# Optimization experiments

Measured on AMD Instinct MI355X. Metric: run time of the kernel, lower is better.

## Reference

```python
import jax, jax.numpy as jnp
import numpy as np
from itertools import combinations_with_replacement

X_SIZE = 6        # dims of x
DEGREE = 2        # moment degree n
NPOINTS = 1_000_000
DIM_V = 28        # comb(X_SIZE + DEGREE, DEGREE)


def _veronese_indices(d, n):
    # monomials of total degree exactly n over homogeneous coords [1, x_1..x_d]
    combos = list(combinations_with_replacement(range(d + 1), n))  # [D_v, n]
    return np.asarray(combos, dtype=np.int32)


def generate_veronese(x, n):
    # x: [dims, npoints] -> v: [D_v, npoints], all monomials of degree <= n in x
    d, N = x.shape
    xh = jnp.concatenate([jnp.ones((1, N), x.dtype), x], axis=0)  # [d+1, N]
    idx = _veronese_indices(d, n)
    v = xh[idx[:, 0]]                 # [D_v, N]
    for k in range(1, n):             # n is tiny (2); fixed small loop
        v = v * xh[idx[:, k]]
    return v


def setup_inputs() -> dict:
    key = jax.random.key(0)
    k1, k2 = jax.random.split(key)
    x = jax.random.normal(k1, (NPOINTS, X_SIZE), dtype=jnp.float32)
    A = jax.random.normal(k2, (DIM_V, DIM_V), dtype=jnp.float32) / DIM_V
    M_inv = A @ A.T + jnp.eye(DIM_V, dtype=jnp.float32)  # SPD, like an inverse moment matrix
    return {"x": x, "M_inv": M_inv, "c": 0}


def reference(x, M_inv, c):
    npoints, dims = x.shape
    # faithful to torch: x.view(dims, npoints) is a reshape, NOT a transpose
    xv = x.reshape(dims, npoints)
    v = generate_veronese(xv, DEGREE)                 # [D_v, N]
    # fused batched quadratic form v^T M_inv v (no BS copies of M_inv)
    q = jnp.einsum('dn,de,en->n', v, M_inv, v)        # [N]
    return q.reshape(npoints, 1, 1)
```

## Files before the change

kernel.cpp:

```cpp
#include <hip/hip_runtime.h>


typedef float f32x2 __attribute__((ext_vector_type(2)));

__global__ void qform2_kernel(const float* __restrict__ x,
                              const float* __restrict__ M,
                              float* __restrict__ out, int N2, int N)
{
    int t = blockIdx.x * blockDim.x + threadIdx.x;
    if (t >= N2) return;
    int n = 2 * t;

    f32x2 xh[7];
    xh[0] = (f32x2){1.0f, 1.0f};
    #pragma unroll
    for (int d = 0; d < 6; ++d)
        xh[d + 1] = *(const f32x2*)(x + (size_t)d * (size_t)N + n);

    f32x2 v[28];
    {
        int vi = 0;
        #pragma unroll
        for (int a = 0; a < 7; ++a)
            #pragma unroll
            for (int b = a; b < 7; ++b)
                v[vi++] = xh[a] * xh[b];
    }

    f32x2 qd = (f32x2){0.0f, 0.0f};
    f32x2 qo = (f32x2){0.0f, 0.0f};
    #pragma unroll
    for (int j = 0; j < 28; ++j) {
        float mjj = M[j * 28 + j];
        f32x2 mjj2 = (f32x2){mjj, mjj};
        qd = __builtin_elementwise_fma(mjj2, v[j] * v[j], qd);
        f32x2 tt = (f32x2){0.0f, 0.0f};
        #pragma unroll
        for (int k = j + 1; k < 28; ++k) {
            float mjk = M[j * 28 + k];
            f32x2 m2 = (f32x2){mjk, mjk};
            tt = __builtin_elementwise_fma(m2, v[k], tt);
        }
        qo = __builtin_elementwise_fma(v[j], tt, qo);
    }
    f32x2 q = __builtin_elementwise_fma((f32x2){2.0f, 2.0f}, qo, qd);
    *(f32x2*)(out + n) = q;
}

extern "C" void kernel_launch(void* const* d_in, const int* in_sizes, int n_in,
                              void* d_out, int out_size, void* d_ws, size_t ws_size,
                              hipStream_t stream)
{
    const float* x   = (const float*)d_in[0];
    const float* M   = (const float*)d_in[1];
    float* out       = (float*)d_out;
    const int N      = out_size;
    const int N2     = N / 2;

    const int block = 256;
    const int grid  = (N2 + block - 1) / block;
    qform2_kernel<<<grid, block, 0, stream>>>(x, M, out, N2, N);
}
```

Before: 15.06 us.

## Prepack doubled upper-triangular M into workspace and split accumulators

Adds a tiny pre-kernel that packs the upper triangle of M into a contiguous 406-float buffer, with the off-diagonal entries pre-doubled. This removes the separate diagonal accumulation and the final scale by two. The main kernel reads the packed coefficients, spreads its accumulation over four independent accumulators to shorten the FMA dependency chain, and adds launch bounds. The cost is an extra kernel launch, plus a dependency on workspace being available.

New measurement: 19.69 us. 30.7% more time.

```diff
diff --git a/kernel.cpp b/kernel.cpp
--- a/kernel.cpp
+++ b/kernel.cpp
@@ -3,9 +3,22 @@
 
 typedef float f32x2 __attribute__((ext_vector_type(2)));
 
-__global__ void qform2_kernel(const float* __restrict__ x,
-                              const float* __restrict__ M,
-                              float* __restrict__ out, int N2, int N)
+__host__ __device__ constexpr int tri_off(int j) { return j * 28 - (j * (j - 1)) / 2; }
+
+__global__ void pack_kernel(const float* __restrict__ M, float* __restrict__ C)
+{
+    int i = blockIdx.x * blockDim.x + threadIdx.x;
+    if (i >= 406) return;
+    int j = 0;
+    while (tri_off(j + 1) <= i) ++j;
+    int k = j + (i - tri_off(j));
+    float m = M[j * 28 + k];
+    C[i] = (k == j) ? m : 2.0f * m;
+}
+
+__global__ __launch_bounds__(256, 4)
+void qform2_kernel(const float* __restrict__ x, const float* __restrict__ C,
+                   float* __restrict__ out, int N2, int N)
 {
     int t = blockIdx.x * blockDim.x + threadIdx.x;
     if (t >= N2) return;
@@ -27,23 +40,22 @@
                 v[vi++] = xh[a] * xh[b];
     }
 
-    f32x2 qd = (f32x2){0.0f, 0.0f};
-    f32x2 qo = (f32x2){0.0f, 0.0f};
+    f32x2 acc[4];
+    #pragma unroll
+    for (int i = 0; i < 4; ++i) acc[i] = (f32x2){0.0f, 0.0f};
+
     #pragma unroll
     for (int j = 0; j < 28; ++j) {
-        float mjj = M[j * 28 + j];
-        f32x2 mjj2 = (f32x2){mjj, mjj};
-        qd = __builtin_elementwise_fma(mjj2, v[j] * v[j], qd);
-        f32x2 tt = (f32x2){0.0f, 0.0f};
+        float cjj = C[tri_off(j)];
+        f32x2 tt = (f32x2){cjj, cjj} * v[j];
         #pragma unroll
         for (int k = j + 1; k < 28; ++k) {
-            float mjk = M[j * 28 + k];
-            f32x2 m2 = (f32x2){mjk, mjk};
-            tt = __builtin_elementwise_fma(m2, v[k], tt);
+            float c = C[tri_off(j) + (k - j)];
+            tt = __builtin_elementwise_fma((f32x2){c, c}, v[k], tt);
         }
-        qo = __builtin_elementwise_fma(v[j], tt, qo);
+        acc[j & 3] = __builtin_elementwise_fma(v[j], tt, acc[j & 3]);
     }
-    f32x2 q = __builtin_elementwise_fma((f32x2){2.0f, 2.0f}, qo, qd);
+    f32x2 q = (acc[0] + acc[1]) + (acc[2] + acc[3]);
     *(f32x2*)(out + n) = q;
 }
 
@@ -54,10 +66,13 @@
     const float* x   = (const float*)d_in[0];
     const float* M   = (const float*)d_in[1];
     float* out       = (float*)d_out;
+    float* C         = (float*)d_ws;
     const int N      = out_size;
     const int N2     = N / 2;
 
+    pack_kernel<<<1, 512, 0, stream>>>(M, C);
+
     const int block = 256;
     const int grid  = (N2 + block - 1) / block;
-    qform2_kernel<<<grid, block, 0, stream>>>(x, M, out, N2, N);
+    qform2_kernel<<<grid, block, 0, stream>>>(x, C, out, N2, N);
 }
```

## Software-pipeline M row loads with inline-asm scalar dwordx16 loads

Applied to the files above, without the earlier changes.

Replaces the compiler-scheduled scalar loads of M with a hand-written recursive template. Each step issues s_load_dwordx16 for the upper-triangle row segment of the next row before computing the current row, so scalar-memory latency overlaps the FMAs. It also adds launch bounds of 256 threads with 5 blocks per SIMD to cap register use. The inline asm, hand-computed offsets and explicit s_waitcnt make the code fragile, and the extra live SGPRs could increase pressure.

Measured after the change: 14.57 us. -3.3%, faster.

```diff
diff --git a/kernel.cpp b/kernel.cpp
--- a/kernel.cpp
+++ b/kernel.cpp
@@ -1,11 +1,64 @@
 #include <hip/hip_runtime.h>
 
 
-typedef float f32x2 __attribute__((ext_vector_type(2)));
+typedef float f32x2  __attribute__((ext_vector_type(2)));
+typedef float f32x16 __attribute__((ext_vector_type(16)));
 
-__global__ void qform2_kernel(const float* __restrict__ x,
-                              const float* __restrict__ M,
-                              float* __restrict__ out, int N2, int N)
+#define ROW_OFF(J)  ((J) == 27 ? 3072 : 116 * (J))
+#define ROW_OFF2(J) (116 * (J) + 64)
+
+template <int J>
+__device__ __forceinline__ void row_step(const float* __restrict__ M,
+                                         const f32x2 (&v)[28],
+                                         f32x2& qd, f32x2& qo,
+                                         f32x16 b0, f32x16 b1)
+{
+    if constexpr (J < 12)
+        asm volatile("s_waitcnt lgkmcnt(0)" : "+s"(b0), "+s"(b1));
+    else
+        asm volatile("s_waitcnt lgkmcnt(0)" : "+s"(b0));
+
+    f32x16 n0{}, n1{};
+    if constexpr (J + 1 < 28) {
+        asm volatile("s_load_dwordx16 %0, %2, %3"
+                     : "=s"(n0), "+s"(b0)
+                     : "s"(M), "i"(ROW_OFF(J + 1)));
+        if constexpr (J + 1 < 12)
+            asm volatile("s_load_dwordx16 %0, %2, %3"
+                         : "=s"(n1), "+s"(b0)
+                         : "s"(M), "i"(ROW_OFF2(J + 1)));
+    }
+
+    constexpr int d0 = (J == 27) ? 15 : 0;
+    {
+        float c = b0[d0];
+        qd = __builtin_elementwise_fma((f32x2){c, c}, v[J] * v[J], qd);
+    }
+    if constexpr (J < 27) {
+        f32x2 t = (f32x2){0.0f, 0.0f};
+        constexpr int n_in_b0 = (27 - J < 15) ? (27 - J) : 15;
+        #pragma unroll
+        for (int i = 1; i <= n_in_b0; ++i) {
+            float c = b0[i];
+            t = __builtin_elementwise_fma((f32x2){c, c}, v[J + i], t);
+        }
+        if constexpr (J < 12) {
+            #pragma unroll
+            for (int i = 0; i <= 11 - J; ++i) {
+                float c = b1[i];
+                t = __builtin_elementwise_fma((f32x2){c, c}, v[J + 16 + i], t);
+            }
+        }
+        qo = __builtin_elementwise_fma(v[J], t, qo);
+    }
+
+    if constexpr (J + 1 < 28)
+        row_step<J + 1>(M, v, qd, qo, n0, n1);
+}
+
+__global__ __launch_bounds__(256, 5)
+void qform2_kernel(const float* __restrict__ x, const float* __restrict__ M,
+                   float* __restrict__ out, int N2, int N)
 {
     int t = blockIdx.x * blockDim.x + threadIdx.x;
     if (t >= N2) return;
@@ -29,20 +82,12 @@
 
     f32x2 qd = (f32x2){0.0f, 0.0f};
     f32x2 qo = (f32x2){0.0f, 0.0f};
-    #pragma unroll
-    for (int j = 0; j < 28; ++j) {
-        float mjj = M[j * 28 + j];
-        f32x2 mjj2 = (f32x2){mjj, mjj};
-        qd = __builtin_elementwise_fma(mjj2, v[j] * v[j], qd);
-        f32x2 tt = (f32x2){0.0f, 0.0f};
-        #pragma unroll
-        for (int k = j + 1; k < 28; ++k) {
-            float mjk = M[j * 28 + k];
-            f32x2 m2 = (f32x2){mjk, mjk};
-            tt = __builtin_elementwise_fma(m2, v[k], tt);
-        }
-        qo = __builtin_elementwise_fma(v[j], tt, qo);
-    }
+
+    f32x16 b0, b1;
+    asm volatile("s_load_dwordx16 %0, %1, 0"  : "=s"(b0) : "s"(M));
+    asm volatile("s_load_dwordx16 %0, %1, 64" : "=s"(b1) : "s"(M));
+    row_step<0>(M, v, qd, qo, b0, b1);
+
     f32x2 q = __builtin_elementwise_fma((f32x2){2.0f, 2.0f}, qo, qd);
     *(f32x2*)(out + n) = q;
 }
```
